# Kernel optimization log

Hardware: AMD Instinct MI355X
Metric: run time of the kernel (lower is better)

## Reference

```python
import jax, jax.numpy as jnp
import numpy as np

NUM_PAGES = 1048576
TOKENS_PER_PAGE = 32
SLOTS = 256
MAX_PAGES_PER_SLOT = 4096
MAX_SEQ = 65536  # <= max_pages_per_slot*tokens_per_page/2, leaves room to grow


def setup_inputs() -> dict:
    key = jax.random.key(0)
    k1, = jax.random.split(key, 1)
    # random current sequence lengths per slot (some may be 0 / inactive)
    seq = jax.random.randint(k1, (SLOTS,), 0, MAX_SEQ).astype(jnp.int32)
    npu = (seq + TOKENS_PER_PAGE - 1) // TOKENS_PER_PAGE  # ceil-div pages used
    cols = jnp.arange(MAX_PAGES_PER_SLOT, dtype=jnp.int32)
    # give slot i the disjoint page-id range [1 + i*2048, ...); valid since
    # max pages/slot here = ceil(65535/32) = 2048 and 1+255*2048+2047 < NUM_PAGES
    pm = jnp.where(
        cols[None, :] < npu[:, None],
        1 + jnp.arange(SLOTS, dtype=jnp.int32)[:, None] * 2048 + cols[None, :],
        -1,
    ).astype(jnp.int32)
    # mark exactly the mapped pages as in-use (index 0 used as a safe dump slot)
    safe_idx = jnp.where(pm > -1, pm, 0)
    vals = (pm > -1).astype(jnp.int32)
    page_status = jnp.zeros((NUM_PAGES,), jnp.int32).at[safe_idx].max(vals)
    page_status = page_status.at[0].set(0)
    current_page = jnp.where(
        npu > 0,
        jnp.take_along_axis(pm, jnp.maximum(npu - 1, 0)[:, None], axis=1)[:, 0],
        -1,
    ).astype(jnp.int32)
    cpp = jnp.where(seq == 0, 0, (seq - 1) % TOKENS_PER_PAGE).astype(jnp.int32)
    return {
        "page_status": page_status,
        "page_map": pm,
        "sequence_lengths": seq,
        "num_pages_used": npu.astype(jnp.int32),
        "current_page": current_page,
        "current_page_position": cpp,
    }


def _find_next_free_page(page_status):
    # matches PageManager.find_next_free_page: first free index in [1, N), else 0
    free = jnp.where(page_status[1:] == 0, size=1, fill_value=-1)[0] + 1
    return free[0].astype(jnp.int32)


def reference(page_status, page_map, sequence_lengths, num_pages_used,
              current_page, current_page_position):
    """Faithful port of PageManager.reserve_decode_step_pages (autoregressive step)."""
    tpp = TOKENS_PER_PAGE
    new_seq = sequence_lengths + jnp.where(current_page == -1, 0, 1).astype(jnp.int32)
    new_npu = (new_seq + tpp - 1) // tpp
    new_cpp = jnp.where(new_seq == 0, 0, (new_seq - 1) % tpp).astype(jnp.int32)

    def step(carry, i):
        ps, pm, cp = carry
        needs_new_page = new_npu[i] > num_pages_used[i]
        nfp = jax.lax.cond(
            needs_new_page,
            lambda: _find_next_free_page(ps),
            lambda: jnp.int32(-1),
        )
        ps = jax.lax.cond(needs_new_page, lambda x: x.at[nfp].set(1), lambda x: x, ps)
        pm = jax.lax.cond(
            needs_new_page,
            lambda x: x.at[i, num_pages_used[i]].set(nfp),
            lambda x: x,
            pm,
        )
        cp = jax.lax.cond(needs_new_page, lambda x: x.at[i].set(nfp), lambda x: x, cp)
        return (ps, pm, cp), None

    (ps, pm, cp), _ = jax.lax.scan(
        step, (page_status, page_map, current_page), jnp.arange(SLOTS, dtype=jnp.int32)
    )
    # PageState fields in declaration order
    return (ps, pm, new_seq, new_npu.astype(jnp.int32), cp, new_cpp)
```

## Files before the change

kernel.cpp:

```cpp
#include <hip/hip_runtime.h>

#define NUM_PAGES 1048576
#define TPP 32
#define SLOTS 256
#define MPPS 4096
#define NBLK 1024
#define NTHR 256
#define NR4 (NUM_PAGES / 1024)


__global__ __launch_bounds__(NTHR) void fused(
    const int* __restrict__ ps, const int* __restrict__ pm,
    const int* __restrict__ seq, const int* __restrict__ npu,
    const int* __restrict__ cp, int* __restrict__ out)
{
    const int t = threadIdx.x, b = blockIdx.x;
    const int lane = t & 63, wave = t >> 6;

    int* out_ps  = out;
    int* out_pm  = out + NUM_PAGES;
    int* out_seq = out + 2 * NUM_PAGES;
    int* out_npu = out_seq + SLOTS;
    int* out_cp  = out_npu + SLOTS;
    int* out_cpp = out_cp + SLOTS;

    __shared__ int s_free[SLOTS];
    __shared__ int s_rank[SLOTS];
    __shared__ int s_cpo[SLOTS];

    const int4* ps4 = reinterpret_cast<const int4*>(ps);
    const int gi = b * NTHR + t;
    const int my_round = 4 * b + wave;

    const int4 sq4 = reinterpret_cast<const int4*>(seq)[lane];
    const int4 cq4 = reinterpret_cast<const int4*>(cp)[lane];
    const int4 nu4 = reinterpret_cast<const int4*>(npu)[lane];
    int4 A = ps4[lane];
    int4 B = ps4[64 + lane];
    int4 C = ps4[128 + lane];
    const int4 pv = ps4[gi];
    const int4 mv = reinterpret_cast<const int4*>(pm)[gi];

    int ns0 = sq4.x + (cq4.x != -1), nn0 = (ns0 + TPP - 1) >> 5;
    int ns1 = sq4.y + (cq4.y != -1), nn1 = (ns1 + TPP - 1) >> 5;
    int ns2 = sq4.z + (cq4.z != -1), nn2 = (ns2 + TPP - 1) >> 5;
    int ns3 = sq4.w + (cq4.w != -1), nn3 = (ns3 + TPP - 1) >> 5;
    int nb = (nn0 > nu4.x ? 1 : 0) | (nn1 > nu4.y ? 2 : 0) |
             (nn2 > nu4.z ? 4 : 0) | (nn3 > nu4.w ? 8 : 0);

    int cnt = __popc(nb), x = cnt;
    #pragma unroll
    for (int o = 1; o < 64; o <<= 1) { int y = __shfl_up(x, o); if (lane >= o) x += y; }
    const int K = __shfl(x, 63);
    const int base_r = x - cnt;
    const int iv0 = (nb & 1) ? base_r : -1;
    const int iv1 = (nb & 2) ? base_r + (nb & 1) : -1;
    const int iv2 = (nb & 4) ? base_r + __popc(nb & 3) : -1;
    const int iv3 = (nb & 8) ? base_r + __popc(nb & 7) : -1;

    if (b == 0 && wave == 0) {
        int4 o;
        o.x = ns0; o.y = ns1; o.z = ns2; o.w = ns3;
        reinterpret_cast<int4*>(out_seq)[lane] = o;
        o.x = nn0; o.y = nn1; o.z = nn2; o.w = nn3;
        reinterpret_cast<int4*>(out_npu)[lane] = o;
        o.x = ns0 ? ((ns0 - 1) & 31) : 0;
        o.y = ns1 ? ((ns1 - 1) & 31) : 0;
        o.z = ns2 ? ((ns2 - 1) & 31) : 0;
        o.w = ns3 ? ((ns3 - 1) & 31) : 0;
        reinterpret_cast<int4*>(out_cpp)[lane] = o;
        o.x = iv0; o.y = iv1; o.z = iv2; o.w = iv3;
        reinterpret_cast<int4*>(s_rank)[lane] = o;
        reinterpret_cast<int4*>(s_cpo)[lane] = cq4;
    }

    const int slot_b = b >> 2;
    const int src_lane = slot_b >> 2;
    const int jb = slot_b & 3;
    int my_iv = (jb == 0) ? iv0 : (jb == 1) ? iv1 : (jb == 2) ? iv2 : iv3;
    int my_nu = (jb == 0) ? nu4.x : (jb == 1) ? nu4.y : (jb == 2) ? nu4.z : nu4.w;
    const int tr    = __shfl(my_iv, src_lane);
    const int col_b = __shfl(my_nu, src_lane);

    int sf = 0, pmask = 0, nfp_pm = -1, r = 0;
    while (sf < K && r < NR4) {
        int4 v = A; A = B; B = C;
        C = (r + 3 < NR4) ? ps4[(r + 3) * 64 + lane] : make_int4(1, 1, 1, 1);
        int m = ((v.x == 0) ? 1 : 0) | ((v.y == 0) ? 2 : 0) |
                ((v.z == 0) ? 4 : 0) | ((v.w == 0) ? 8 : 0);
        if (r == 0 && lane == 0) m &= ~1;
        int q = __popc(m), xx = q;
        #pragma unroll
        for (int o = 1; o < 64; o <<= 1) { int y = __shfl_up(xx, o); if (lane >= o) xx += y; }
        int pos = sf + xx - q;
        int p0 = pos;
        int p1 = pos + (m & 1);
        int p2 = pos + __popc(m & 3);
        int p3 = pos + __popc(m & 7);
        int pg = r * 256 + lane * 4;
        if (r == my_round) {
            if ((m & 1) && p0 < K) pmask |= 1;
            if ((m & 2) && p1 < K) pmask |= 2;
            if ((m & 4) && p2 < K) pmask |= 4;
            if ((m & 8) && p3 < K) pmask |= 8;
        }
        if (b == 0) {
            if ((m & 1) && p0 < K) s_free[p0] = pg;
            if ((m & 2) && p1 < K) s_free[p1] = pg + 1;
            if ((m & 4) && p2 < K) s_free[p2] = pg + 2;
            if ((m & 8) && p3 < K) s_free[p3] = pg + 3;
        }
        if (tr >= 0 && nfp_pm < 0) {
            int fl = -1;
            if ((m & 1) && p0 == tr) fl = pg;
            if ((m & 2) && p1 == tr) fl = pg + 1;
            if ((m & 4) && p2 == tr) fl = pg + 2;
            if ((m & 8) && p3 == tr) fl = pg + 3;
            unsigned long long bb = __ballot(fl >= 0);
            if (bb) nfp_pm = __shfl(fl, __ffsll(bb) - 1);
        }
        sf += __shfl(xx, 63);
        ++r;
    }
    const int fe = (sf < K) ? sf : K;

    int4 opv = pv, omv = mv;
    if (gi == 0 && fe < K) pmask |= 1;
    if (pmask & 1) opv.x = 1;
    if (pmask & 2) opv.y = 1;
    if (pmask & 4) opv.z = 1;
    if (pmask & 8) opv.w = 1;
    if (tr >= 0) {
        int nfp = (tr < fe) ? nfp_pm : 0;
        int d = col_b - ((b & 3) << 10) - (t << 2);
        if (d == 0) omv.x = nfp;
        else if (d == 1) omv.y = nfp;
        else if (d == 2) omv.z = nfp;
        else if (d == 3) omv.w = nfp;
    }
    reinterpret_cast<int4*>(out_ps)[gi] = opv;
    reinterpret_cast<int4*>(out_pm)[gi] = omv;

    if (b == 0) {
        __syncthreads();
        int rk = s_rank[t];
        out_cp[t] = (rk >= 0) ? ((rk < fe) ? s_free[rk] : 0) : s_cpo[t];
    }
}

extern "C" void kernel_launch(void* const* d_in, const int* in_sizes, int n_in,
                              void* d_out, int out_size, void* d_ws, size_t ws_size,
                              hipStream_t stream)
{
    const int* page_status = (const int*)d_in[0];
    const int* page_map    = (const int*)d_in[1];
    const int* seq         = (const int*)d_in[2];
    const int* npu         = (const int*)d_in[3];
    const int* cp          = (const int*)d_in[4];

    fused<<<NBLK, NTHR, 0, stream>>>(
        page_status, page_map, seq, npu, cp, (int*)d_out);
}
```

Measured before the change: 12.42 us.

## Scan free pages with whole block in 1024-page chunks instead of per-wave rounds

Replaces the sequential per-wave scan over 256-page rounds with a block-wide scan: all four waves evaluate three 1024-page chunks up front, combine wave prefix sums through shared memory, and fall back to a chunked loop with block barriers only if more free pages are needed. The point is to shorten the serial dependency chain of the free-page search, which dominates latency in this tiny kernel. It adds __syncthreads barriers and shared-memory traffic, and moves the per-slot found page into a shared variable written by any thread.

New measurement: 10.47 us. -15.7%, faster.

```diff
diff --git a/kernel.cpp b/kernel.cpp
--- a/kernel.cpp
+++ b/kernel.cpp
@@ -6,8 +6,6 @@
 #define MPPS 4096
 #define NBLK 1024
 #define NTHR 256
-#define NR4 (NUM_PAGES / 1024)
-
 
 __global__ __launch_bounds__(NTHR) void fused(
     const int* __restrict__ ps, const int* __restrict__ pm,
@@ -24,22 +22,25 @@
     int* out_cp  = out_npu + SLOTS;
     int* out_cpp = out_cp + SLOTS;
 
+    __shared__ int s_w[12];
     __shared__ int s_free[SLOTS];
     __shared__ int s_rank[SLOTS];
     __shared__ int s_cpo[SLOTS];
+    __shared__ int s_pmval;
 
     const int4* ps4 = reinterpret_cast<const int4*>(ps);
     const int gi = b * NTHR + t;
-    const int my_round = 4 * b + wave;
 
     const int4 sq4 = reinterpret_cast<const int4*>(seq)[lane];
     const int4 cq4 = reinterpret_cast<const int4*>(cp)[lane];
     const int4 nu4 = reinterpret_cast<const int4*>(npu)[lane];
-    int4 A = ps4[lane];
-    int4 B = ps4[64 + lane];
-    int4 C = ps4[128 + lane];
-    const int4 pv = ps4[gi];
-    const int4 mv = reinterpret_cast<const int4*>(pm)[gi];
+    const int4 pc0 = ps4[t];
+    const int4 pc1 = ps4[NTHR + t];
+    const int4 pc2 = ps4[2 * NTHR + t];
+    int4 pv = ps4[gi];
+    int4 mv = reinterpret_cast<const int4*>(pm)[gi];
+
+    if (t == 0) s_pmval = 0;
 
     int ns0 = sq4.x + (cq4.x != -1), nn0 = (ns0 + TPP - 1) >> 5;
     int ns1 = sq4.y + (cq4.y != -1), nn1 = (ns1 + TPP - 1) >> 5;
@@ -47,7 +48,6 @@
     int ns3 = sq4.w + (cq4.w != -1), nn3 = (ns3 + TPP - 1) >> 5;
     int nb = (nn0 > nu4.x ? 1 : 0) | (nn1 > nu4.y ? 2 : 0) |
              (nn2 > nu4.z ? 4 : 0) | (nn3 > nu4.w ? 8 : 0);
-
     int cnt = __popc(nb), x = cnt;
     #pragma unroll
     for (int o = 1; o < 64; o <<= 1) { int y = __shfl_up(x, o); if (lane >= o) x += y; }
@@ -75,74 +75,114 @@
     }
 
     const int slot_b = b >> 2;
-    const int src_lane = slot_b >> 2;
     const int jb = slot_b & 3;
     int my_iv = (jb == 0) ? iv0 : (jb == 1) ? iv1 : (jb == 2) ? iv2 : iv3;
     int my_nu = (jb == 0) ? nu4.x : (jb == 1) ? nu4.y : (jb == 2) ? nu4.z : nu4.w;
-    const int tr    = __shfl(my_iv, src_lane);
-    const int col_b = __shfl(my_nu, src_lane);
-
-    int sf = 0, pmask = 0, nfp_pm = -1, r = 0;
-    while (sf < K && r < NR4) {
-        int4 v = A; A = B; B = C;
-        C = (r + 3 < NR4) ? ps4[(r + 3) * 64 + lane] : make_int4(1, 1, 1, 1);
-        int m = ((v.x == 0) ? 1 : 0) | ((v.y == 0) ? 2 : 0) |
-                ((v.z == 0) ? 4 : 0) | ((v.w == 0) ? 8 : 0);
-        if (r == 0 && lane == 0) m &= ~1;
+    const int tr    = __shfl(my_iv, slot_b >> 2);
+    const int col_b = __shfl(my_nu, slot_b >> 2);
+
+    auto fm = [](int4 v) {
+        return ((v.x == 0) ? 1 : 0) | ((v.y == 0) ? 2 : 0) |
+               ((v.z == 0) ? 4 : 0) | ((v.w == 0) ? 8 : 0);
+    };
+    int m0 = fm(pc0), m1 = fm(pc1), m2 = fm(pc2);
+    if (t == 0) m0 &= ~1;
+    int q0 = __popc(m0), q1 = __popc(m1), q2 = __popc(m2);
+    int x0 = q0, x1 = q1, x2 = q2;
+    #pragma unroll
+    for (int o = 1; o < 64; o <<= 1) {
+        int y0 = __shfl_up(x0, o), y1 = __shfl_up(x1, o), y2 = __shfl_up(x2, o);
+        if (lane >= o) { x0 += y0; x1 += y1; x2 += y2; }
+    }
+    if (lane == 63) { s_w[wave] = x0; s_w[4 + wave] = x1; s_w[8 + wave] = x2; }
+    __syncthreads();
+    int w0 = 0, w1 = 0, w2 = 0, T0 = 0, T1 = 0, T2 = 0;
+    #pragma unroll
+    for (int w = 0; w < 4; ++w) {
+        int a0 = s_w[w], a1 = s_w[4 + w], a2 = s_w[8 + w];
+        if (w < wave) { w0 += a0; w1 += a1; w2 += a2; }
+        T0 += a0; T1 += a1; T2 += a2;
+    }
+    const int pos0 = w0 + x0 - q0;
+    const int pos1 = T0 + w1 + x1 - q1;
+    const int pos2 = T0 + T1 + w2 + x2 - q2;
+    const int fe_fast = T0 + T1 + T2;
+
+    if (b == 0) {
+        #pragma unroll
+        for (int j = 0; j < 4; ++j) {
+            if (m0 & (1 << j)) { int p = pos0 + __popc(m0 & ((1 << j) - 1)); if (p < K) s_free[p] = t * 4 + j; }
+            if (m1 & (1 << j)) { int p = pos1 + __popc(m1 & ((1 << j) - 1)); if (p < K) s_free[p] = 1024 + t * 4 + j; }
+            if (m2 & (1 << j)) { int p = pos2 + __popc(m2 & ((1 << j) - 1)); if (p < K) s_free[p] = 2048 + t * 4 + j; }
+        }
+    }
+    if (tr >= 0) {
+        int fl = -1;
+        #pragma unroll
+        for (int j = 0; j < 4; ++j) {
+            if (m0 & (1 << j)) { if (pos0 + __popc(m0 & ((1 << j) - 1)) == tr) fl = t * 4 + j; }
+            if (m1 & (1 << j)) { if (pos1 + __popc(m1 & ((1 << j) - 1)) == tr) fl = 1024 + t * 4 + j; }
+            if (m2 & (1 << j)) { if (pos2 + __popc(m2 & ((1 << j) - 1)) == tr) fl = 2048 + t * 4 + j; }
+        }
+        if (fl >= 0) s_pmval = fl;
+    }
+
+    int pmask = 0;
+    if (b < 3) {
+        int mm = (b == 0) ? m0 : (b == 1) ? m1 : m2;
+        int pp = (b == 0) ? pos0 : (b == 1) ? pos1 : pos2;
+        #pragma unroll
+        for (int j = 0; j < 4; ++j)
+            if (mm & (1 << j)) { int p = pp + __popc(mm & ((1 << j) - 1)); if (p < K) pmask |= 1 << j; }
+    }
+
+    int fe_total = fe_fast;
+    for (int ch = 3; (ch << 10) < NUM_PAGES && fe_total < K; ++ch) {
+        int4 v = ps4[(ch << 8) + t];
+        int m = fm(v);
         int q = __popc(m), xx = q;
         #pragma unroll
         for (int o = 1; o < 64; o <<= 1) { int y = __shfl_up(xx, o); if (lane >= o) xx += y; }
-        int pos = sf + xx - q;
-        int p0 = pos;
-        int p1 = pos + (m & 1);
-        int p2 = pos + __popc(m & 3);
-        int p3 = pos + __popc(m & 7);
-        int pg = r * 256 + lane * 4;
-        if (r == my_round) {
-            if ((m & 1) && p0 < K) pmask |= 1;
-            if ((m & 2) && p1 < K) pmask |= 2;
-            if ((m & 4) && p2 < K) pmask |= 4;
-            if ((m & 8) && p3 < K) pmask |= 8;
+        if (lane == 63) s_w[wave] = xx;
+        __syncthreads();
+        int wo = 0, T = 0;
+        #pragma unroll
+        for (int w = 0; w < 4; ++w) { if (w < wave) wo += s_w[w]; T += s_w[w]; }
+        int pos = fe_total + wo + xx - q;
+        #pragma unroll
+        for (int j = 0; j < 4; ++j) if (m & (1 << j)) {
+            int p = pos + __popc(m & ((1 << j) - 1));
+            if (p < K) {
+                int pg = (ch << 10) + (t << 2) + j;
+                if (b == 0) s_free[p] = pg;
+                if (p == tr) s_pmval = pg;
+                if (b == ch) pmask |= 1 << j;
+            }
         }
-        if (b == 0) {
-            if ((m & 1) && p0 < K) s_free[p0] = pg;
-            if ((m & 2) && p1 < K) s_free[p1] = pg + 1;
-            if ((m & 4) && p2 < K) s_free[p2] = pg + 2;
-            if ((m & 8) && p3 < K) s_free[p3] = pg + 3;
-        }
-        if (tr >= 0 && nfp_pm < 0) {
-            int fl = -1;
-            if ((m & 1) && p0 == tr) fl = pg;
-            if ((m & 2) && p1 == tr) fl = pg + 1;
-            if ((m & 4) && p2 == tr) fl = pg + 2;
-            if ((m & 8) && p3 == tr) fl = pg + 3;
-            unsigned long long bb = __ballot(fl >= 0);
-            if (bb) nfp_pm = __shfl(fl, __ffsll(bb) - 1);
-        }
-        sf += __shfl(xx, 63);
-        ++r;
-    }
-    const int fe = (sf < K) ? sf : K;
-
-    int4 opv = pv, omv = mv;
-    if (gi == 0 && fe < K) pmask |= 1;
-    if (pmask & 1) opv.x = 1;
-    if (pmask & 2) opv.y = 1;
-    if (pmask & 4) opv.z = 1;
-    if (pmask & 8) opv.w = 1;
+        fe_total += T;
+        __syncthreads();
+    }
+    const int fe = (fe_total < K) ? fe_total : K;
+    if (K > fe_total && gi == 0) pmask |= 1;
+
+    __syncthreads();
+
+    if (pmask & 1) pv.x = 1;
+    if (pmask & 2) pv.y = 1;
+    if (pmask & 4) pv.z = 1;
+    if (pmask & 8) pv.w = 1;
     if (tr >= 0) {
-        int nfp = (tr < fe) ? nfp_pm : 0;
+        int nfp = (tr < fe) ? s_pmval : 0;
         int d = col_b - ((b & 3) << 10) - (t << 2);
-        if (d == 0) omv.x = nfp;
-        else if (d == 1) omv.y = nfp;
-        else if (d == 2) omv.z = nfp;
-        else if (d == 3) omv.w = nfp;
-    }
-    reinterpret_cast<int4*>(out_ps)[gi] = opv;
-    reinterpret_cast<int4*>(out_pm)[gi] = omv;
+        if (d == 0) mv.x = nfp;
+        else if (d == 1) mv.y = nfp;
+        else if (d == 2) mv.z = nfp;
+        else if (d == 3) mv.w = nfp;
+    }
+    reinterpret_cast<int4*>(out_ps)[gi] = pv;
+    reinterpret_cast<int4*>(out_pm)[gi] = mv;
 
     if (b == 0) {
-        __syncthreads();
         int rk = s_rank[t];
         out_cp[t] = (rk >= 0) ? ((rk < fe) ? s_free[rk] : 0) : s_cpo[t];
     }
```
